# Optimization experiments

Hardware: AMD Instinct MI355X
Metric: run time of the kernel (lower is better)

The kernel has to match this reference:

```python
import jax, jax.numpy as jnp
import numpy as np


def _depthwise3x3(x_nhwc, w):
    # w: (3, 3, 1, C) — depthwise conv, padding=1, matches torch Conv2d(groups=C)
    return jax.lax.conv_general_dilated(
        x_nhwc, w, window_strides=(1, 1), padding='SAME',
        dimension_numbers=('NHWC', 'HWIO', 'NHWC'),
        feature_group_count=x_nhwc.shape[-1])


def _stripe_attn(q, k, v, lepe_w, B, H, W, nh, hd, ss, axis, scale):
    # q/k/v: (B, H, W, nh*hd); axis 0 = horizontal stripes, 1 = vertical
    pad_h = (-H) % ss if axis == 0 else 0
    pad_w = (-W) % ss if axis == 1 else 0
    if pad_h or pad_w:
        pad = ((0, 0), (0, pad_h), (0, pad_w), (0, 0))
        q, k, v = jnp.pad(q, pad), jnp.pad(k, pad), jnp.pad(v, pad)
    Hp, Wp = q.shape[1], q.shape[2]
    lepe = _depthwise3x3(v, lepe_w)  # (B, Hp, Wp, nh*hd)

    if axis == 0:
        nS = Hp // ss
        def to_win(t):  # -> (B*nS*Wp, nh, ss, hd)
            t = t.reshape(B, nS, ss, Wp, nh, hd)
            return t.transpose(0, 1, 3, 4, 2, 5).reshape(B * nS * Wp, nh, ss, hd)
    else:
        nS = Wp // ss
        def to_win(t):  # -> (B*Hp*nS, nh, ss, hd)
            t = t.reshape(B, Hp, nS, ss, nh, hd)
            return t.transpose(0, 1, 2, 4, 3, 5).reshape(B * Hp * nS, nh, ss, hd)

    qw, kw, vw, lw = to_win(q), to_win(k), to_win(v), to_win(lepe)
    attn = jax.nn.softmax(jnp.einsum('wnqd,wnkd->wnqk', qw, kw) / scale, axis=-1)
    out = jnp.einsum('wnqk,wnkd->wnqd', attn, vw) + lw  # (Wnum, nh, ss, hd)

    if axis == 0:
        out = out.transpose(0, 2, 1, 3).reshape(B, nS, Wp, ss, nh * hd)
        out = out.transpose(0, 1, 3, 2, 4).reshape(B, Hp, Wp, nh * hd)
    else:
        out = out.transpose(0, 2, 1, 3).reshape(B, Hp, nS, ss, nh * hd)
        out = out.reshape(B, Hp, Wp, nh * hd)
    return out[:, :H, :W, :].reshape(B, H * W, nh * hd)


def setup_inputs() -> dict:
    key = jax.random.key(0)
    ks = jax.random.split(key, 6)
    B, H, W, dim, n_heads, ss = 8, 64, 64, 512, 16, 8
    half = dim // 2
    x = jax.random.normal(ks[0], (B, H * W, dim), dtype=jnp.float32)
    w_qkv = jax.random.normal(ks[1], (3 * dim, dim), dtype=jnp.float32) * 0.02
    w_proj = jax.random.normal(ks[2], (dim, dim), dtype=jnp.float32) * 0.02
    b_proj = jnp.zeros((dim,), dtype=jnp.float32)
    lepe_h_w = jax.random.normal(ks[3], (3, 3, 1, half), dtype=jnp.float32) * 0.1
    lepe_v_w = jax.random.normal(ks[4], (3, 3, 1, half), dtype=jnp.float32) * 0.1
    return {"x": x, "w_qkv": w_qkv, "w_proj": w_proj, "b_proj": b_proj,
            "lepe_h_w": lepe_h_w, "lepe_v_w": lepe_v_w, "H": H, "W": W}


def reference(x, w_qkv, w_proj, b_proj, lepe_h_w, lepe_v_w, H, W):
    B, L, C = x.shape
    n_heads, ss = 16, 8
    hd = C // n_heads
    scale = float(np.sqrt(hd))
    qkv = x @ w_qkv.T  # (B, L, 3C)
    q, k, v = jnp.split(qkv, 3, axis=-1)
    q = q.reshape(B, H, W, C)
    k = k.reshape(B, H, W, C)
    v = v.reshape(B, H, W, C)
    half = C // 2
    nh_h = n_heads // 2
    nh_v = n_heads - nh_h
    out_h = _stripe_attn(q[..., :half], k[..., :half], v[..., :half],
                         lepe_h_w, B, H, W, nh_h, hd, ss, axis=0, scale=scale)
    out_v = _stripe_attn(q[..., half:], k[..., half:], v[..., half:],
                         lepe_v_w, B, H, W, nh_v, hd, ss, axis=1, scale=scale)
    out = jnp.concatenate([out_h, out_v], axis=-1)
    return out @ w_proj.T + b_proj
```

## Files before the change

kernel.cpp:

```cpp
#include <hip/hip_runtime.h>
#include <hip/hip_bf16.h>
#include <stdint.h>

typedef _Float16 half2v __attribute__((ext_vector_type(2)));
typedef _Float16 half8v __attribute__((ext_vector_type(8)));
typedef uint32_t u32x4  __attribute__((ext_vector_type(4)));
typedef float    f32x4  __attribute__((ext_vector_type(4)));

__device__ __forceinline__ unsigned short f2h(float f) {
  _Float16 h = (_Float16)f;
  return __builtin_bit_cast(unsigned short, h);
}
__device__ __forceinline__ half2v bch2(uint32_t u) {
  return __builtin_bit_cast(half2v, u);
}
__device__ __forceinline__ uint32_t pkrtz_u32(float a, float b) {
  return __builtin_bit_cast(uint32_t, __builtin_amdgcn_cvt_pkrtz(a, b));
}

__device__ __forceinline__ int qkv_idx(int half, int b, int n, int h, int w) {
  int idx = half * 8388608 + (b * 8 + n) * 131072;
  idx += (half == 0) ? ((h >> 3) * 16384 + w * 256 + (h & 7) * 32)
                     : (h * 2048 + w * 32);
  return idx;
}

#define GLOAD_LDS16(gsrc, lbase)                                          \
  __builtin_amdgcn_global_load_lds(                                       \
      (const __attribute__((address_space(1))) uint32_t*)(gsrc),          \
      (__attribute__((address_space(3))) uint32_t*)(lbase), 16, 0, 0)

__global__ __launch_bounds__(256) void cvt_f32_f16(const float* __restrict__ in,
                                                   unsigned short* __restrict__ out,
                                                   int n4) {
  int i = blockIdx.x * 256 + threadIdx.x;
  if (i >= n4) return;
  float4 f = reinterpret_cast<const float4*>(in)[i];
  ushort4 u;
  u.x = f2h(f.x); u.y = f2h(f.y); u.z = f2h(f.z); u.w = f2h(f.w);
  reinterpret_cast<ushort4*>(out)[i] = u;
}

template<int MODE>
__global__ __launch_bounds__(256) void gemm_bt(
    const unsigned short* __restrict__ A,
    const unsigned short* __restrict__ B,
    unsigned short* __restrict__ Cq,
    float* __restrict__ Cf,
    const float* __restrict__ bias,
    int M, int N, int K)
{
  __shared__ unsigned short As[2][128 * 32];
  __shared__ unsigned short Bs[2][128 * 32];
  const int tid  = threadIdx.x;
  const int gn   = N >> 7;
  const int cpx  = gridDim.x >> 3;
  const int bid  = blockIdx.x;
  const int wgid = (bid & 7) * cpx + (bid >> 3);
  const int m0   = (wgid / gn) * 128;
  const int n0   = (wgid % gn) * 128;
  const int wave = tid >> 6, lane = tid & 63;
  const int wr = wave >> 1, wc = wave & 1;
  const int sr = tid >> 2;
  const int sc = ((tid & 3) ^ ((tid >> 3) & 3)) * 8;
  const size_t aBase0 = (size_t)(m0 + sr) * K + sc;
  const size_t aBase1 = (size_t)(m0 + 64 + sr) * K + sc;
  const size_t bBase0 = (size_t)(n0 + sr) * K + sc;
  const size_t bBase1 = (size_t)(n0 + 64 + sr) * K + sc;
  char* ldsA = (char*)(&As[0][0]) + (tid & ~63) * 16;
  char* ldsB = (char*)(&Bs[0][0]) + (tid & ~63) * 16;

#define STAGE_TILE(bsel, kofs)                                  \
  do {                                                          \
    GLOAD_LDS16(A + aBase0 + (kofs), ldsA + (bsel) * 8192);     \
    GLOAD_LDS16(A + aBase1 + (kofs), ldsA + (bsel) * 8192 + 4096); \
    GLOAD_LDS16(B + bBase0 + (kofs), ldsB + (bsel) * 8192);     \
    GLOAD_LDS16(B + bBase1 + (kofs), ldsB + (bsel) * 8192 + 4096); \
  } while (0)

  STAGE_TILE(0, 0);

  f32x4 acc[4][4];
  const f32x4 zero = {0.f, 0.f, 0.f, 0.f};
  #pragma unroll
  for (int i = 0; i < 4; ++i)
    #pragma unroll
    for (int j = 0; j < 4; ++j) acc[i][j] = zero;

  const int lr   = lane & 15;
  const int slot = (lane >> 4) ^ ((lr >> 1) & 3);

  auto compute = [&](const unsigned short* Asb, const unsigned short* Bsb) {
    half8v af[4], bfr[4];
    #pragma unroll
    for (int i = 0; i < 4; ++i)
      af[i] = *reinterpret_cast<const half8v*>(Asb + (wr * 64 + i * 16 + lr) * 32 + slot * 8);
    #pragma unroll
    for (int j = 0; j < 4; ++j)
      bfr[j] = *reinterpret_cast<const half8v*>(Bsb + (wc * 64 + j * 16 + lr) * 32 + slot * 8);
    __builtin_amdgcn_s_setprio(1);
    #pragma unroll
    for (int i = 0; i < 4; ++i)
      #pragma unroll
      for (int j = 0; j < 4; ++j)
        acc[i][j] = __builtin_amdgcn_mfma_f32_16x16x32_f16(bfr[j], af[i], acc[i][j], 0, 0, 0);
    __builtin_amdgcn_s_setprio(0);
  };

  const int nt = K >> 5;
  for (int t = 0; t < nt - 1; ++t) {
    STAGE_TILE((t + 1) & 1, (t + 1) * 32);
    asm volatile("s_waitcnt vmcnt(4)" ::: "memory");
    __builtin_amdgcn_s_barrier();
    __builtin_amdgcn_sched_barrier(0);
    compute(&As[t & 1][0], &Bs[t & 1][0]);
    __builtin_amdgcn_s_barrier();
    __builtin_amdgcn_sched_barrier(0);
  }
  asm volatile("s_waitcnt vmcnt(0)" ::: "memory");
  __builtin_amdgcn_s_barrier();
  __builtin_amdgcn_sched_barrier(0);
  compute(&As[(nt - 1) & 1][0], &Bs[(nt - 1) & 1][0]);
#undef STAGE_TILE

  const int cr = (lane >> 4) * 4;
  const int cc = lane & 15;

  if constexpr (MODE == 0) {
    #pragma unroll
    for (int j = 0; j < 4; ++j) {
      const int n = n0 + wc * 64 + j * 16 + cr;
      const float4 b4 = *reinterpret_cast<const float4*>(bias + n);
      #pragma unroll
      for (int i = 0; i < 4; ++i) {
        const int m = m0 + wr * 64 + i * 16 + cc;
        float4 r;
        r.x = acc[i][j][0] + b4.x;
        r.y = acc[i][j][1] + b4.y;
        r.z = acc[i][j][2] + b4.z;
        r.w = acc[i][j][3] + b4.w;
        *reinterpret_cast<float4*>(Cf + (size_t)m * N + n) = r;
      }
    }
  } else {
    const int mb   = m0 + wr * 64;
    const int btok = mb >> 12;
    const int htok = (mb >> 6) & 63;
    #pragma unroll
    for (int j = 0; j < 4; ++j) {
      const int nb    = n0 + wc * 64 + j * 16 + cr;
      const int tq    = nb >> 9;
      const int halfc = (nb >> 8) & 1;
      const int nn    = (nb & 255) >> 5;
      const int ch4   = nb & 31;
      int base = tq * 16777216 + halfc * 8388608 + (btok * 8 + nn) * 131072 + ch4;
      base += halfc ? (htok * 2048) : ((htok >> 3) * 16384 + (htok & 7) * 32);
      const int wstride = halfc ? 32 : 256;
      #pragma unroll
      for (int i = 0; i < 4; ++i) {
        const int wpix = i * 16 + cc;
        uint2 r;
        r.x = pkrtz_u32(acc[i][j][0], acc[i][j][1]);
        r.y = pkrtz_u32(acc[i][j][2], acc[i][j][3]);
        *reinterpret_cast<uint2*>(Cq + base + wpix * wstride) = r;
      }
    }
  }
}

__global__ __launch_bounds__(256) void attn_lepe(
    const unsigned short* __restrict__ qkvp,
    const unsigned short* __restrict__ wlep,
    unsigned short* __restrict__ outp)
{
  const int gw   = (int)((blockIdx.x * 256 + threadIdx.x) >> 6);
  const int lane = threadIdx.x & 63;
  const int half = gw >> 14;
  const int id   = gw & 16383;
  const int b    = id >> 11;
  const int n    = (id >> 8) & 7;
  int h0, w0;
  if (half == 0) { h0 = ((id >> 5) & 7) * 8; w0 = (id & 31) * 2; }
  else           { h0 = ((id >> 3) & 31) * 2; w0 = (id & 7) * 8; }
  const int baseA = qkv_idx(half, b, n, h0, w0);
  const int dWin  = (half == 0) ? 256 : 2048;
  const int baseB = baseA + dWin;

  const int qr = lane >> 3, kr = lane & 7;
  const unsigned short* qA = qkvp + baseA + qr * 32;
  const unsigned short* kA = qkvp + 16777216 + baseA + kr * 32;
  float sA = 0.f, sB = 0.f;
  #pragma unroll
  for (int c = 0; c < 4; ++c) {
    const u32x4 qa = *reinterpret_cast<const u32x4*>(qA + c * 8);
    const u32x4 ka = *reinterpret_cast<const u32x4*>(kA + c * 8);
    const u32x4 qb = *reinterpret_cast<const u32x4*>(qA + dWin + c * 8);
    const u32x4 kb = *reinterpret_cast<const u32x4*>(kA + dWin + c * 8);
    #pragma unroll
    for (int e = 0; e < 4; ++e) {
      sA = __builtin_amdgcn_fdot2(bch2(qa[e]), bch2(ka[e]), sA, false);
      sB = __builtin_amdgcn_fdot2(bch2(qb[e]), bch2(kb[e]), sB, false);
    }
  }
  const float scl = 0.17677669529663687f;
  const float pA = __expf(sA * scl);
  const float pB = __expf(sB * scl);
  float denA = pA, denB = pB;
  denA += __shfl_xor(denA, 1); denA += __shfl_xor(denA, 2); denA += __shfl_xor(denA, 4);
  denB += __shfl_xor(denB, 1); denB += __shfl_xor(denB, 2); denB += __shfl_xor(denB, 4);
  const float aAv = pA * __builtin_amdgcn_rcpf(denA);
  const float aBv = pB * __builtin_amdgcn_rcpf(denB);
  const uint32_t adu = pkrtz_u32(aAv, aBv);

  const int dgrp = lane & 3;
  const int win  = (lane >> 2) & 1;
  const int qr2  = lane >> 3;
  const int d0   = dgrp * 8;
  const int mybase = win ? baseB : baseA;
  const unsigned short* vwin = qkvp + 33554432 + mybase;

  half2v o01 = {0,0}, o23 = {0,0}, o45 = {0,0}, o67 = {0,0};
  #pragma unroll
  for (int k = 0; k < 8; ++k) {
    const uint32_t pairw = (uint32_t)__shfl((int)adu, qr2 * 8 + k);
    const half2v ph = bch2(pairw);
    const _Float16 av = win ? ph.y : ph.x;
    const half2v ak2 = {av, av};
    const u32x4 vv = *reinterpret_cast<const u32x4*>(vwin + k * 32 + d0);
    o01 += ak2 * bch2(vv[0]);
    o23 += ak2 * bch2(vv[1]);
    o45 += ak2 * bch2(vv[2]);
    o67 += ak2 * bch2(vv[3]);
  }

  const int hq = (half == 0) ? (h0 + qr2) : (h0 + win);
  const int wq = (half == 0) ? (w0 + win) : (w0 + qr2);
  const unsigned short* vplane = qkvp + 33554432;
  const unsigned short* wl = wlep + half * 2304 + n * 32 + d0;
  half2v l01 = {0,0}, l23 = {0,0}, l45 = {0,0}, l67 = {0,0};
  #pragma unroll
  for (int dy = -1; dy <= 1; ++dy) {
    #pragma unroll
    for (int dx = -1; dx <= 1; ++dx) {
      const int hh = hq + dy, ww = wq + dx;
      u32x4 vv = {0u, 0u, 0u, 0u};
      if ((unsigned)hh < 64u && (unsigned)ww < 64u)
        vv = *reinterpret_cast<const u32x4*>(vplane + qkv_idx(half, b, n, hh, ww) + d0);
      const u32x4 wt = *reinterpret_cast<const u32x4*>(wl + ((dy + 1) * 3 + dx + 1) * 256);
      l01 += bch2(wt[0]) * bch2(vv[0]);
      l23 += bch2(wt[1]) * bch2(vv[1]);
      l45 += bch2(wt[2]) * bch2(vv[2]);
      l67 += bch2(wt[3]) * bch2(vv[3]);
    }
  }

  const int m = b * 4096 + hq * 64 + wq;
  const int chan0 = half * 256 + n * 32;
  u32x4 r;
  r[0] = __builtin_bit_cast(uint32_t, (half2v)(o01 + l01));
  r[1] = __builtin_bit_cast(uint32_t, (half2v)(o23 + l23));
  r[2] = __builtin_bit_cast(uint32_t, (half2v)(o45 + l45));
  r[3] = __builtin_bit_cast(uint32_t, (half2v)(o67 + l67));
  *reinterpret_cast<u32x4*>(outp + (size_t)m * 512 + chan0 + d0) = r;
}

extern "C" void kernel_launch(void* const* d_in, const int* in_sizes, int n_in,
                              void* d_out, int out_size, void* d_ws, size_t ws_size,
                              hipStream_t stream) {
  const float* x      = (const float*)d_in[0];
  const float* w_qkv  = (const float*)d_in[1];
  const float* w_proj = (const float*)d_in[2];
  const float* b_proj = (const float*)d_in[3];
  const float* lepe_h = (const float*)d_in[4];
  const float* lepe_v = (const float*)d_in[5];
  float* out = (float*)d_out;

  char* ws = (char*)d_ws;
  unsigned short* qkv_p   = (unsigned short*)ws;
  unsigned short* xh      = (unsigned short*)(ws + 100663296);
  unsigned short* wqkv_h  = (unsigned short*)(ws + 134217728);
  unsigned short* wproj_h = (unsigned short*)(ws + 135790592);
  unsigned short* wlep_h  = (unsigned short*)(ws + 136314880);

  cvt_f32_f16<<<16384, 256, 0, stream>>>(x, xh, 4194304);
  cvt_f32_f16<<<768,   256, 0, stream>>>(w_qkv, wqkv_h, 196608);
  cvt_f32_f16<<<256,   256, 0, stream>>>(w_proj, wproj_h, 65536);
  cvt_f32_f16<<<3,     256, 0, stream>>>(lepe_h, wlep_h, 576);
  cvt_f32_f16<<<3,     256, 0, stream>>>(lepe_v, wlep_h + 2304, 576);

  gemm_bt<1><<<3072, 256, 0, stream>>>(
      xh, wqkv_h, qkv_p, nullptr, nullptr, 32768, 1536, 512);

  attn_lepe<<<8192, 256, 0, stream>>>(qkv_p, wlep_h, xh);

  gemm_bt<0><<<1024, 256, 0, stream>>>(
      xh, wproj_h, nullptr, out, b_proj, 32768, 512, 512);
}
```

Before: 184.2 us.

## Enlarge GEMM tiles to 256x256 with 8 waves and 4-stage LDS pipeline

Both GEMMs now use 256x256 output tiles computed by 512-thread workgroups, where each wave owns 128x64 of the output. Global-to-LDS loads are prefetched three stages ahead through a 4-deep ring buffer, with waitcnt levels tuned for the pipeline tail. The intent is more data reuse per LDS byte and better hiding of memory latency. The cost is 128 KB of LDS per block, twice the accumulators per thread, and far fewer blocks: 256 for the projection GEMM, which may underfill 256 CUs. Occupancy and register pressure could also suffer.

```diff
diff --git a/kernel.cpp b/kernel.cpp
--- a/kernel.cpp
+++ b/kernel.cpp
@@ -42,7 +42,7 @@
 }
 
 template<int MODE>
-__global__ __launch_bounds__(256) void gemm_bt(
+__global__ __launch_bounds__(512, 2) void gemm_bt(
     const unsigned short* __restrict__ A,
     const unsigned short* __restrict__ B,
     unsigned short* __restrict__ Cq,
@@ -50,40 +50,43 @@
     const float* __restrict__ bias,
     int M, int N, int K)
 {
-  __shared__ unsigned short As[2][128 * 32];
-  __shared__ unsigned short Bs[2][128 * 32];
+  __shared__ unsigned short As[4][256 * 32];
+  __shared__ unsigned short Bs[4][256 * 32];
   const int tid  = threadIdx.x;
-  const int gn   = N >> 7;
+  const int gn   = N >> 8;
   const int cpx  = gridDim.x >> 3;
   const int bid  = blockIdx.x;
   const int wgid = (bid & 7) * cpx + (bid >> 3);
-  const int m0   = (wgid / gn) * 128;
-  const int n0   = (wgid % gn) * 128;
+  const int m0   = (wgid / gn) * 256;
+  const int n0   = (wgid % gn) * 256;
   const int wave = tid >> 6, lane = tid & 63;
-  const int wr = wave >> 1, wc = wave & 1;
+  const int wr  = wave >> 2;
+  const int wcn = wave & 3;
   const int sr = tid >> 2;
   const int sc = ((tid & 3) ^ ((tid >> 3) & 3)) * 8;
   const size_t aBase0 = (size_t)(m0 + sr) * K + sc;
-  const size_t aBase1 = (size_t)(m0 + 64 + sr) * K + sc;
+  const size_t aBase1 = (size_t)(m0 + 128 + sr) * K + sc;
   const size_t bBase0 = (size_t)(n0 + sr) * K + sc;
-  const size_t bBase1 = (size_t)(n0 + 64 + sr) * K + sc;
+  const size_t bBase1 = (size_t)(n0 + 128 + sr) * K + sc;
   char* ldsA = (char*)(&As[0][0]) + (tid & ~63) * 16;
   char* ldsB = (char*)(&Bs[0][0]) + (tid & ~63) * 16;
 
-#define STAGE_TILE(bsel, kofs)                                  \
-  do {                                                          \
-    GLOAD_LDS16(A + aBase0 + (kofs), ldsA + (bsel) * 8192);     \
-    GLOAD_LDS16(A + aBase1 + (kofs), ldsA + (bsel) * 8192 + 4096); \
-    GLOAD_LDS16(B + bBase0 + (kofs), ldsB + (bsel) * 8192);     \
-    GLOAD_LDS16(B + bBase1 + (kofs), ldsB + (bsel) * 8192 + 4096); \
+#define STAGE_TILE(bsel, kofs)                                      \
+  do {                                                              \
+    GLOAD_LDS16(A + aBase0 + (kofs), ldsA + (bsel) * 16384);        \
+    GLOAD_LDS16(A + aBase1 + (kofs), ldsA + (bsel) * 16384 + 8192); \
+    GLOAD_LDS16(B + bBase0 + (kofs), ldsB + (bsel) * 16384);        \
+    GLOAD_LDS16(B + bBase1 + (kofs), ldsB + (bsel) * 16384 + 8192); \
   } while (0)
 
   STAGE_TILE(0, 0);
-
-  f32x4 acc[4][4];
+  STAGE_TILE(1, 32);
+  STAGE_TILE(2, 64);
+
+  f32x4 acc[8][4];
   const f32x4 zero = {0.f, 0.f, 0.f, 0.f};
   #pragma unroll
-  for (int i = 0; i < 4; ++i)
+  for (int i = 0; i < 8; ++i)
     #pragma unroll
     for (int j = 0; j < 4; ++j) acc[i][j] = zero;
 
@@ -91,36 +94,36 @@
   const int slot = (lane >> 4) ^ ((lr >> 1) & 3);
 
   auto compute = [&](const unsigned short* Asb, const unsigned short* Bsb) {
-    half8v af[4], bfr[4];
-    #pragma unroll
-    for (int i = 0; i < 4; ++i)
-      af[i] = *reinterpret_cast<const half8v*>(Asb + (wr * 64 + i * 16 + lr) * 32 + slot * 8);
+    half8v bf[4];
     #pragma unroll
     for (int j = 0; j < 4; ++j)
-      bfr[j] = *reinterpret_cast<const half8v*>(Bsb + (wc * 64 + j * 16 + lr) * 32 + slot * 8);
+      bf[j] = *reinterpret_cast<const half8v*>(Bsb + (wcn * 64 + j * 16 + lr) * 32 + slot * 8);
+    half8v af[8];
+    #pragma unroll
+    for (int i = 0; i < 8; ++i)
+      af[i] = *reinterpret_cast<const half8v*>(Asb + (wr * 128 + i * 16 + lr) * 32 + slot * 8);
     __builtin_amdgcn_s_setprio(1);
     #pragma unroll
-    for (int i = 0; i < 4; ++i)
+    for (int i = 0; i < 8; ++i)
       #pragma unroll
       for (int j = 0; j < 4; ++j)
-        acc[i][j] = __builtin_amdgcn_mfma_f32_16x16x32_f16(bfr[j], af[i], acc[i][j], 0, 0, 0);
+        acc[i][j] = __builtin_amdgcn_mfma_f32_16x16x32_f16(bf[j], af[i], acc[i][j], 0, 0, 0);
     __builtin_amdgcn_s_setprio(0);
   };
 
   const int nt = K >> 5;
-  for (int t = 0; t < nt - 1; ++t) {
-    STAGE_TILE((t + 1) & 1, (t + 1) * 32);
-    asm volatile("s_waitcnt vmcnt(4)" ::: "memory");
+  for (int t = 0; t < nt; ++t) {
+    if (t + 3 < nt) STAGE_TILE((t + 3) & 3, (t + 3) * 32);
+    if (t < nt - 3)       asm volatile("s_waitcnt vmcnt(12)" ::: "memory");
+    else if (t == nt - 3) asm volatile("s_waitcnt vmcnt(8)"  ::: "memory");
+    else if (t == nt - 2) asm volatile("s_waitcnt vmcnt(4)"  ::: "memory");
+    else                  asm volatile("s_waitcnt vmcnt(0)"  ::: "memory");
     __builtin_amdgcn_s_barrier();
     __builtin_amdgcn_sched_barrier(0);
-    compute(&As[t & 1][0], &Bs[t & 1][0]);
+    compute(&As[t & 3][0], &Bs[t & 3][0]);
     __builtin_amdgcn_s_barrier();
     __builtin_amdgcn_sched_barrier(0);
   }
-  asm volatile("s_waitcnt vmcnt(0)" ::: "memory");
-  __builtin_amdgcn_s_barrier();
-  __builtin_amdgcn_sched_barrier(0);
-  compute(&As[(nt - 1) & 1][0], &Bs[(nt - 1) & 1][0]);
 #undef STAGE_TILE
 
   const int cr = (lane >> 4) * 4;
@@ -129,11 +132,11 @@
   if constexpr (MODE == 0) {
     #pragma unroll
     for (int j = 0; j < 4; ++j) {
-      const int n = n0 + wc * 64 + j * 16 + cr;
+      const int n = n0 + wcn * 64 + j * 16 + cr;
       const float4 b4 = *reinterpret_cast<const float4*>(bias + n);
       #pragma unroll
-      for (int i = 0; i < 4; ++i) {
-        const int m = m0 + wr * 64 + i * 16 + cc;
+      for (int i = 0; i < 8; ++i) {
+        const int m = m0 + wr * 128 + i * 16 + cc;
         float4 r;
         r.x = acc[i][j][0] + b4.x;
         r.y = acc[i][j][1] + b4.y;
@@ -143,26 +146,28 @@
       }
     }
   } else {
-    const int mb   = m0 + wr * 64;
+    const int mb   = m0 + wr * 128;
     const int btok = mb >> 12;
-    const int htok = (mb >> 6) & 63;
+    const int hr0  = (mb >> 6) & 63;
     #pragma unroll
     for (int j = 0; j < 4; ++j) {
-      const int nb    = n0 + wc * 64 + j * 16 + cr;
+      const int nb    = n0 + wcn * 64 + j * 16 + cr;
       const int tq    = nb >> 9;
       const int halfc = (nb >> 8) & 1;
       const int nn    = (nb & 255) >> 5;
       const int ch4   = nb & 31;
-      int base = tq * 16777216 + halfc * 8388608 + (btok * 8 + nn) * 131072 + ch4;
-      base += halfc ? (htok * 2048) : ((htok >> 3) * 16384 + (htok & 7) * 32);
-      const int wstride = halfc ? 32 : 256;
+      const int headbase = tq * 16777216 + halfc * 8388608 +
+                           (btok * 8 + nn) * 131072 + ch4;
       #pragma unroll
-      for (int i = 0; i < 4; ++i) {
-        const int wpix = i * 16 + cc;
+      for (int i = 0; i < 8; ++i) {
+        const int hrow = hr0 + (i >> 2);
+        const int wpix = (i & 3) * 16 + cc;
+        const int off = halfc ? (hrow * 2048 + wpix * 32)
+                              : ((hrow >> 3) * 16384 + wpix * 256 + (hrow & 7) * 32);
         uint2 r;
         r.x = pkrtz_u32(acc[i][j][0], acc[i][j][1]);
         r.y = pkrtz_u32(acc[i][j][2], acc[i][j][3]);
-        *reinterpret_cast<uint2*>(Cq + base + wpix * wstride) = r;
+        *reinterpret_cast<uint2*>(Cq + headbase + off) = r;
       }
     }
   }
@@ -288,11 +293,11 @@
   cvt_f32_f16<<<3,     256, 0, stream>>>(lepe_h, wlep_h, 576);
   cvt_f32_f16<<<3,     256, 0, stream>>>(lepe_v, wlep_h + 2304, 576);
 
-  gemm_bt<1><<<3072, 256, 0, stream>>>(
+  gemm_bt<1><<<768, 512, 0, stream>>>(
       xh, wqkv_h, qkv_p, nullptr, nullptr, 32768, 1536, 512);
 
   attn_lepe<<<8192, 256, 0, stream>>>(qkv_p, wlep_h, xh);
 
-  gemm_bt<0><<<1024, 256, 0, stream>>>(
+  gemm_bt<0><<<256, 512, 0, stream>>>(
       xh, wproj_h, nullptr, out, b_proj, 32768, 512, 512);
 }
```

Result: slower. 192.9 us (+4.7%).

## Fuse fp32-to-fp16 conversion of input into the QKV GEMM loader

Applied to the files above, without the earlier changes.

Removes the standalone conversion pass over x and has the QKV GEMM stream fp32 tiles of x into LDS directly, converting them to fp16 in registers before the MFMAs. This removes a full read/write pass over the activation and its intermediate buffer. In exchange the GEMM moves twice the A bytes per tile, uses more LDS, and repeats the conversion for every N tile. The templated GEMM is split into two specialized kernels with constant shapes.

```diff
diff --git a/kernel.cpp b/kernel.cpp
--- a/kernel.cpp
+++ b/kernel.cpp
@@ -41,15 +41,133 @@
   reinterpret_cast<ushort4*>(out)[i] = u;
 }
 
-template<int MODE>
-__global__ __launch_bounds__(256) void gemm_bt(
+__global__ __launch_bounds__(256) void gemm_qkv(
+    const float* __restrict__ X,
+    const unsigned short* __restrict__ B,
+    unsigned short* __restrict__ Cq)
+{
+  constexpr int K = 512, N = 1536;
+  __shared__ float          Af[2][128 * 32];
+  __shared__ unsigned short Bh[2][128 * 32];
+  const int tid  = threadIdx.x;
+  const int gn   = N >> 7;
+  const int cpx  = gridDim.x >> 3;
+  const int bid  = blockIdx.x;
+  const int wgid = (bid & 7) * cpx + (bid >> 3);
+  const int m0   = (wgid / gn) * 128;
+  const int n0   = (wgid % gn) * 128;
+  const int wave = tid >> 6, lane = tid & 63;
+  const int wr = wave >> 1, wc = wave & 1;
+  const int sr  = tid >> 2;
+  const int scB = ((tid & 3) ^ ((tid >> 3) & 3)) * 8;
+  const size_t bBase0 = (size_t)(n0 + sr) * K + scB;
+  const size_t bBase1 = (size_t)(n0 + 64 + sr) * K + scB;
+  const int arow = tid >> 3;
+  const int acsw = ((tid & 7) ^ (arow & 7)) * 4;
+  const size_t aBase = (size_t)(m0 + arow) * K + acsw;
+  char* ldsA = (char*)(&Af[0][0]) + (tid & ~63) * 16;
+  char* ldsB = (char*)(&Bh[0][0]) + (tid & ~63) * 16;
+
+#define STAGE_Q(bsel, kt)                                                \
+  do {                                                                   \
+    GLOAD_LDS16(X + aBase + (kt),            ldsA + (bsel) * 16384);     \
+    GLOAD_LDS16(X + aBase + 32 * K + (kt),   ldsA + (bsel) * 16384 + 4096); \
+    GLOAD_LDS16(X + aBase + 64 * K + (kt),   ldsA + (bsel) * 16384 + 8192); \
+    GLOAD_LDS16(X + aBase + 96 * K + (kt),   ldsA + (bsel) * 16384 + 12288);\
+    GLOAD_LDS16(B + bBase0 + (kt),           ldsB + (bsel) * 8192);      \
+    GLOAD_LDS16(B + bBase1 + (kt),           ldsB + (bsel) * 8192 + 4096);  \
+  } while (0)
+
+  STAGE_Q(0, 0);
+
+  f32x4 acc[4][4];
+  const f32x4 zero = {0.f, 0.f, 0.f, 0.f};
+  #pragma unroll
+  for (int i = 0; i < 4; ++i)
+    #pragma unroll
+    for (int j = 0; j < 4; ++j) acc[i][j] = zero;
+
+  const int lr    = lane & 15;
+  const int kg    = lane >> 4;
+  const int slotB = kg ^ ((lr >> 1) & 3);
+  const int pA0   = (2 * kg)     ^ (lr & 7);
+  const int pA1   = (2 * kg + 1) ^ (lr & 7);
+
+  auto compute = [&](const float* Asb, const unsigned short* Bsb) {
+    half8v bfr[4], af[4];
+    #pragma unroll
+    for (int j = 0; j < 4; ++j)
+      bfr[j] = *reinterpret_cast<const half8v*>(Bsb + (wc * 64 + j * 16 + lr) * 32 + slotB * 8);
+    #pragma unroll
+    for (int i = 0; i < 4; ++i) {
+      const float* rowp = Asb + (wr * 64 + i * 16 + lr) * 32;
+      const float4 fa = *reinterpret_cast<const float4*>(rowp + pA0 * 4);
+      const float4 fb = *reinterpret_cast<const float4*>(rowp + pA1 * 4);
+      u32x4 pk;
+      pk[0] = pkrtz_u32(fa.x, fa.y);
+      pk[1] = pkrtz_u32(fa.z, fa.w);
+      pk[2] = pkrtz_u32(fb.x, fb.y);
+      pk[3] = pkrtz_u32(fb.z, fb.w);
+      af[i] = __builtin_bit_cast(half8v, pk);
+    }
+    __builtin_amdgcn_s_setprio(1);
+    #pragma unroll
+    for (int i = 0; i < 4; ++i)
+      #pragma unroll
+      for (int j = 0; j < 4; ++j)
+        acc[i][j] = __builtin_amdgcn_mfma_f32_16x16x32_f16(bfr[j], af[i], acc[i][j], 0, 0, 0);
+    __builtin_amdgcn_s_setprio(0);
+  };
+
+  const int nt = K >> 5;
+  for (int t = 0; t < nt - 1; ++t) {
+    STAGE_Q((t + 1) & 1, (t + 1) * 32);
+    asm volatile("s_waitcnt vmcnt(6)" ::: "memory");
+    __builtin_amdgcn_s_barrier();
+    __builtin_amdgcn_sched_barrier(0);
+    compute(&Af[t & 1][0], &Bh[t & 1][0]);
+    __builtin_amdgcn_s_barrier();
+    __builtin_amdgcn_sched_barrier(0);
+  }
+  asm volatile("s_waitcnt vmcnt(0)" ::: "memory");
+  __builtin_amdgcn_s_barrier();
+  __builtin_amdgcn_sched_barrier(0);
+  compute(&Af[(nt - 1) & 1][0], &Bh[(nt - 1) & 1][0]);
+#undef STAGE_Q
+
+  const int cr = (lane >> 4) * 4;
+  const int cc = lane & 15;
+  const int mb   = m0 + wr * 64;
+  const int btok = mb >> 12;
+  const int htok = (mb >> 6) & 63;
+  #pragma unroll
+  for (int j = 0; j < 4; ++j) {
+    const int nb    = n0 + wc * 64 + j * 16 + cr;
+    const int tq    = nb >> 9;
+    const int halfc = (nb >> 8) & 1;
+    const int nn    = (nb & 255) >> 5;
+    const int ch4   = nb & 31;
+    int base = tq * 16777216 + halfc * 8388608 + (btok * 8 + nn) * 131072 + ch4;
+    base += halfc ? (htok * 2048) : ((htok >> 3) * 16384 + (htok & 7) * 32);
+    const int wstride = halfc ? 32 : 256;
+    #pragma unroll
+    for (int i = 0; i < 4; ++i) {
+      const int wpix = i * 16 + cc;
+      uint2 r;
+      r.x = pkrtz_u32(acc[i][j][0], acc[i][j][1]);
+      r.y = pkrtz_u32(acc[i][j][2], acc[i][j][3]);
+      *reinterpret_cast<uint2*>(Cq + base + wpix * wstride) = r;
+    }
+  }
+}
+
+__global__ __launch_bounds__(256) void gemm_proj(
     const unsigned short* __restrict__ A,
     const unsigned short* __restrict__ B,
-    unsigned short* __restrict__ Cq,
     float* __restrict__ Cf,
-    const float* __restrict__ bias,
-    int M, int N, int K)
+    const float* __restrict__ bias)
 {
+  constexpr int K = 512, N = 512;
   __shared__ unsigned short As[2][128 * 32];
   __shared__ unsigned short Bs[2][128 * 32];
   const int tid  = threadIdx.x;
@@ -70,15 +188,15 @@
   char* ldsA = (char*)(&As[0][0]) + (tid & ~63) * 16;
   char* ldsB = (char*)(&Bs[0][0]) + (tid & ~63) * 16;
 
-#define STAGE_TILE(bsel, kofs)                                  \
-  do {                                                          \
-    GLOAD_LDS16(A + aBase0 + (kofs), ldsA + (bsel) * 8192);     \
+#define STAGE_P(bsel, kofs)                                        \
+  do {                                                             \
+    GLOAD_LDS16(A + aBase0 + (kofs), ldsA + (bsel) * 8192);        \
     GLOAD_LDS16(A + aBase1 + (kofs), ldsA + (bsel) * 8192 + 4096); \
-    GLOAD_LDS16(B + bBase0 + (kofs), ldsB + (bsel) * 8192);     \
+    GLOAD_LDS16(B + bBase0 + (kofs), ldsB + (bsel) * 8192);        \
     GLOAD_LDS16(B + bBase1 + (kofs), ldsB + (bsel) * 8192 + 4096); \
   } while (0)
 
-  STAGE_TILE(0, 0);
+  STAGE_P(0, 0);
 
   f32x4 acc[4][4];
   const f32x4 zero = {0.f, 0.f, 0.f, 0.f};
@@ -109,7 +227,7 @@
 
   const int nt = K >> 5;
   for (int t = 0; t < nt - 1; ++t) {
-    STAGE_TILE((t + 1) & 1, (t + 1) * 32);
+    STAGE_P((t + 1) & 1, (t + 1) * 32);
     asm volatile("s_waitcnt vmcnt(4)" ::: "memory");
     __builtin_amdgcn_s_barrier();
     __builtin_amdgcn_sched_barrier(0);
@@ -121,49 +239,23 @@
   __builtin_amdgcn_s_barrier();
   __builtin_amdgcn_sched_barrier(0);
   compute(&As[(nt - 1) & 1][0], &Bs[(nt - 1) & 1][0]);
-#undef STAGE_TILE
+#undef STAGE_P
 
   const int cr = (lane >> 4) * 4;
   const int cc = lane & 15;
-
-  if constexpr (MODE == 0) {
-    #pragma unroll
-    for (int j = 0; j < 4; ++j) {
-      const int n = n0 + wc * 64 + j * 16 + cr;
-      const float4 b4 = *reinterpret_cast<const float4*>(bias + n);
-      #pragma unroll
-      for (int i = 0; i < 4; ++i) {
-        const int m = m0 + wr * 64 + i * 16 + cc;
-        float4 r;
-        r.x = acc[i][j][0] + b4.x;
-        r.y = acc[i][j][1] + b4.y;
-        r.z = acc[i][j][2] + b4.z;
-        r.w = acc[i][j][3] + b4.w;
-        *reinterpret_cast<float4*>(Cf + (size_t)m * N + n) = r;
-      }
-    }
-  } else {
-    const int mb   = m0 + wr * 64;
-    const int btok = mb >> 12;
-    const int htok = (mb >> 6) & 63;
-    #pragma unroll
-    for (int j = 0; j < 4; ++j) {
-      const int nb    = n0 + wc * 64 + j * 16 + cr;
-      const int tq    = nb >> 9;
-      const int halfc = (nb >> 8) & 1;
-      const int nn    = (nb & 255) >> 5;
-      const int ch4   = nb & 31;
-      int base = tq * 16777216 + halfc * 8388608 + (btok * 8 + nn) * 131072 + ch4;
-      base += halfc ? (htok * 2048) : ((htok >> 3) * 16384 + (htok & 7) * 32);
-      const int wstride = halfc ? 32 : 256;
-      #pragma unroll
-      for (int i = 0; i < 4; ++i) {
-        const int wpix = i * 16 + cc;
-        uint2 r;
-        r.x = pkrtz_u32(acc[i][j][0], acc[i][j][1]);
-        r.y = pkrtz_u32(acc[i][j][2], acc[i][j][3]);
-        *reinterpret_cast<uint2*>(Cq + base + wpix * wstride) = r;
-      }
+  #pragma unroll
+  for (int j = 0; j < 4; ++j) {
+    const int n = n0 + wc * 64 + j * 16 + cr;
+    const float4 b4 = *reinterpret_cast<const float4*>(bias + n);
+    #pragma unroll
+    for (int i = 0; i < 4; ++i) {
+      const int m = m0 + wr * 64 + i * 16 + cc;
+      float4 r;
+      r.x = acc[i][j][0] + b4.x;
+      r.y = acc[i][j][1] + b4.y;
+      r.z = acc[i][j][2] + b4.z;
+      r.w = acc[i][j][3] + b4.w;
+      *reinterpret_cast<float4*>(Cf + (size_t)m * N + n) = r;
     }
   }
 }
@@ -277,22 +369,19 @@
 
   char* ws = (char*)d_ws;
   unsigned short* qkv_p   = (unsigned short*)ws;
-  unsigned short* xh      = (unsigned short*)(ws + 100663296);
+  unsigned short* ah      = (unsigned short*)(ws + 100663296);
   unsigned short* wqkv_h  = (unsigned short*)(ws + 134217728);
   unsigned short* wproj_h = (unsigned short*)(ws + 135790592);
   unsigned short* wlep_h  = (unsigned short*)(ws + 136314880);
 
-  cvt_f32_f16<<<16384, 256, 0, stream>>>(x, xh, 4194304);
-  cvt_f32_f16<<<768,   256, 0, stream>>>(w_qkv, wqkv_h, 196608);
-  cvt_f32_f16<<<256,   256, 0, stream>>>(w_proj, wproj_h, 65536);
-  cvt_f32_f16<<<3,     256, 0, stream>>>(lepe_h, wlep_h, 576);
-  cvt_f32_f16<<<3,     256, 0, stream>>>(lepe_v, wlep_h + 2304, 576);
-
-  gemm_bt<1><<<3072, 256, 0, stream>>>(
-      xh, wqkv_h, qkv_p, nullptr, nullptr, 32768, 1536, 512);
-
-  attn_lepe<<<8192, 256, 0, stream>>>(qkv_p, wlep_h, xh);
-
-  gemm_bt<0><<<1024, 256, 0, stream>>>(
-      xh, wproj_h, nullptr, out, b_proj, 32768, 512, 512);
-}
+  cvt_f32_f16<<<768, 256, 0, stream>>>(w_qkv, wqkv_h, 196608);
+  cvt_f32_f16<<<256, 256, 0, stream>>>(w_proj, wproj_h, 65536);
+  cvt_f32_f16<<<3,   256, 0, stream>>>(lepe_h, wlep_h, 576);
+  cvt_f32_f16<<<3,   256, 0, stream>>>(lepe_v, wlep_h + 2304, 576);
+
+  gemm_qkv<<<3072, 256, 0, stream>>>(x, wqkv_h, qkv_p);
+
+  attn_lepe<<<8192, 256, 0, stream>>>(qkv_p, wlep_h, ah);
+
+  gemm_proj<<<1024, 256, 0, stream>>>(ah, wproj_h, out, b_proj);
+}
```

Result: no change. 187.0 us (+1.5%).
